# Kernel tuning notes

Measured on AMD Instinct MI355X. Metric: run time of the kernel, lower is better.

The kernel has to match this reference:

```python
import jax, jax.numpy as jnp
import numpy as np

D = 256          # embedding_dim
N_SUPPORT = 320  # n_way * n_shot = 20 * 16
N_QUERY = 2048
N_WAY = 20


def setup_inputs() -> dict:
    key = jax.random.key(0)
    ks = jax.random.split(key, 6)
    scale = 1.0 / np.sqrt(2 * D)
    return {
        "support_embeddings": jax.random.normal(ks[0], (N_SUPPORT, D), dtype=jnp.float32),
        "query_embeddings": jax.random.normal(ks[1], (N_QUERY, D), dtype=jnp.float32),
        "support_labels": jax.random.randint(ks[2], (N_SUPPORT,), 0, N_WAY, dtype=jnp.int64)
            if jax.config.jax_enable_x64 else jax.random.randint(ks[2], (N_SUPPORT,), 0, N_WAY, dtype=jnp.int32),
        "W1": jax.random.normal(ks[3], (2 * D, D), dtype=jnp.float32) * scale,
        "b1": jax.random.normal(ks[4], (D,), dtype=jnp.float32) * scale,
        "W2": jax.random.normal(ks[5], (D,), dtype=jnp.float32) * (1.0 / np.sqrt(D)),
        "b2": jnp.zeros((1,), dtype=jnp.float32),
        "n_way": N_WAY,
        "n_shot": 16,
    }


def reference(support_embeddings, query_embeddings, support_labels, W1, b1, W2, b2, n_way, n_shot):
    d = support_embeddings.shape[-1]
    # Linear1 over concat([query, support]) == query @ W1[:d] + support @ W1[d:]
    q_proj = query_embeddings @ W1[:d]          # [Q, D]
    s_proj = support_embeddings @ W1[d:]        # [S, D]
    hidden = jax.nn.relu(q_proj[:, None, :] + s_proj[None, :, :] + b1)  # [Q, S, D]
    scores = jnp.einsum("qsd,d->qs", hidden, W2) + b2[0]                # [Q, S]
    weights = jax.nn.softmax(scores, axis=1)                            # softmax over support set
    onehot = jax.nn.one_hot(support_labels, n_way, dtype=weights.dtype) # [S, n_way]
    logits = weights @ onehot                                           # [Q, n_way]
    return logits
```

## Files before the change

kernel.cpp:

```cpp
#include <hip/hip_runtime.h>
#include <cstdint>

#define DD   256
#define NS   320
#define NQ   2048
#define NWAY 20
#define QTP  8
#define QT   4
#define NQB  (NQ / QTP)
#define NSB  (NS / QTP)
#define CMAX 64

__global__ __launch_bounds__(1024) void proj_kernel(
    const float* __restrict__ sup, const float* __restrict__ qe,
    const float* __restrict__ W1, const float* __restrict__ b1,
    float* __restrict__ qp, float* __restrict__ spbT) {
  __shared__ float pacc[3][QTP][DD];
  const int t  = threadIdx.x;
  const int d  = t & 255;
  const int kq = t >> 8;
  const int b  = blockIdx.x;
  const bool isQ = (b < NQB);
  const int r0 = isQ ? b * QTP : (b - NQB) * QTP;
  const float* src   = isQ ? qe : sup;
  const float* wcol  = W1 + (isQ ? 0 : (size_t)DD * DD) + (size_t)(kq * 64) * DD + d;
  const float* rbase = src + __builtin_amdgcn_readfirstlane(r0 * DD + kq * 64);

  float acc[QTP] = {0.f, 0.f, 0.f, 0.f, 0.f, 0.f, 0.f, 0.f};
#pragma unroll 8
  for (int k = 0; k < 64; ++k) {
    const float wv = wcol[(size_t)k * DD];
#pragma unroll
    for (int i = 0; i < QTP; ++i)
      acc[i] += rbase[i * DD + k] * wv;
  }
  if (kq) {
#pragma unroll
    for (int i = 0; i < QTP; ++i) pacc[kq - 1][i][d] = acc[i];
  }
  __syncthreads();
  if (kq == 0) {
    if (isQ) {
#pragma unroll
      for (int i = 0; i < QTP; ++i)
        qp[(size_t)(r0 + i) * DD + d] =
            acc[i] + pacc[0][i][d] + pacc[1][i][d] + pacc[2][i][d];
    } else {
      const float bb = b1[d];
#pragma unroll
      for (int i = 0; i < QTP; ++i)
        spbT[d * NS + r0 + i] =
            acc[i] + pacc[0][i][d] + pacc[1][i][d] + pacc[2][i][d] + bb;
    }
  }
}

__global__ __launch_bounds__(640) void matchnet_kernel(
    const float* __restrict__ qp, const float* __restrict__ spbT,
    const float* __restrict__ W2, const int* __restrict__ labels,
    float* __restrict__ out) {
  __shared__ float wexp[QT][NS];
  __shared__ float wm[5];
  __shared__ float csum[QT * NWAY];
  __shared__ int   ccnt[NWAY];
  __shared__ short cidx[NWAY * CMAX];
  const int t    = threadIdx.x;
  const int q0   = blockIdx.x * QT;
  const int half = t / NS;
  const int s    = t - half * NS;

  if (t < NWAY) ccnt[t] = 0;
  __syncthreads();
  if (!half) {
    const int lab  = labels[s];
    const int slot = atomicAdd(&ccnt[lab], 1);
    cidx[lab * CMAX + slot] = (short)s;
  }

  const int d0 = half * (DD / 2);
  const float* qb = qp + __builtin_amdgcn_readfirstlane(q0 * DD + d0);
  const float* wb = W2 + d0;
  const float* sb = spbT + (size_t)d0 * NS + s;

  float acc[QT] = {0.f, 0.f, 0.f, 0.f};
#pragma unroll 4
  for (int dd = 0; dd < DD / 2; dd += 4) {
    const float sv0 = sb[(dd + 0) * NS];
    const float sv1 = sb[(dd + 1) * NS];
    const float sv2 = sb[(dd + 2) * NS];
    const float sv3 = sb[(dd + 3) * NS];
    const float4 wv = *(const float4*)(wb + dd);
#pragma unroll
    for (int i = 0; i < QT; ++i) {
      const float4 qv = *(const float4*)(qb + i * DD + dd);
      acc[i] += fmaxf(qv.x + sv0, 0.f) * wv.x
              + fmaxf(qv.y + sv1, 0.f) * wv.y
              + fmaxf(qv.z + sv2, 0.f) * wv.z
              + fmaxf(qv.w + sv3, 0.f) * wv.w;
    }
  }

  if (half) {
#pragma unroll
    for (int i = 0; i < QT; ++i) wexp[i][s] = acc[i];
  }
  __syncthreads();
  float m = -1e30f;
  if (!half) {
#pragma unroll
    for (int i = 0; i < QT; ++i) { acc[i] += wexp[i][s]; m = fmaxf(m, acc[i]); }
#pragma unroll
    for (int off = 32; off > 0; off >>= 1)
      m = fmaxf(m, __shfl_xor(m, off));
    if ((t & 63) == 0) wm[t >> 6] = m;
  }
  __syncthreads();
  if (!half) {
    const float M = fmaxf(fmaxf(fmaxf(wm[0], wm[1]), fmaxf(wm[2], wm[3])), wm[4]);
#pragma unroll
    for (int i = 0; i < QT; ++i) wexp[i][s] = __expf(acc[i] - M);
  }
  __syncthreads();
  if (t < QT * NWAY) {
    const int i = t / NWAY, c = t - i * NWAY;
    const int n = ccnt[c];
    float sum = 0.f;
    for (int j = 0; j < n; ++j) sum += wexp[i][cidx[c * CMAX + j]];
    csum[t] = sum;
  }
  __syncthreads();
  if (t < QT * NWAY) {
    const int i = t / NWAY, c = t - i * NWAY;
    float tot = 0.f;
#pragma unroll
    for (int j = 0; j < NWAY; ++j) tot += csum[i * NWAY + j];
    out[(size_t)(q0 + i) * NWAY + c] = csum[t] / tot;
  }
}

extern "C" void kernel_launch(void* const* d_in, const int* in_sizes, int n_in,
                              void* d_out, int out_size, void* d_ws, size_t ws_size,
                              hipStream_t stream) {
  const float* sup = (const float*)d_in[0];
  const float* qe  = (const float*)d_in[1];
  const int*   lab = (const int*)d_in[2];
  const float* W1  = (const float*)d_in[3];
  const float* b1  = (const float*)d_in[4];
  const float* W2  = (const float*)d_in[5];
  float* out  = (float*)d_out;
  float* spbT = (float*)d_ws;
  float* qpr  = spbT + (size_t)DD * NS;

  proj_kernel<<<NQB + NSB, 1024, 0, stream>>>(sup, qe, W1, b1, qpr, spbT);
  matchnet_kernel<<<NQ / QT, 640, 0, stream>>>(qpr, spbT, W2, lab, out);
}
```

Baseline: 101.0 us.

## Store projections in fp16 and use packed fp16 add/max with fdot2 in matchnet

```diff
diff --git a/kernel.cpp b/kernel.cpp
--- a/kernel.cpp
+++ b/kernel.cpp
@@ -11,10 +11,29 @@
 #define NSB  (NS / QTP)
 #define CMAX 64
 
+typedef _Float16 f16x2 __attribute__((ext_vector_type(2)));
+
+__device__ __forceinline__ f16x2 u2f(unsigned u) {
+  f16x2 f; __builtin_memcpy(&f, &u, 4); return f;
+}
+
+__device__ __forceinline__ float relu_dot2(f16x2 q, f16x2 s, f16x2 w, float c) {
+  f16x2 h = q + s;
+  const f16x2 z = {(_Float16)0.f, (_Float16)0.f};
+  h = __builtin_elementwise_max(h, z);
+#if __has_builtin(__builtin_amdgcn_fdot2)
+  return __builtin_amdgcn_fdot2(h, w, c, false);
+#else
+  return c + (float)h.x * (float)w.x + (float)h.y * (float)w.y;
+#endif
+}
+
 __global__ __launch_bounds__(1024) void proj_kernel(
     const float* __restrict__ sup, const float* __restrict__ qe,
     const float* __restrict__ W1, const float* __restrict__ b1,
-    float* __restrict__ qp, float* __restrict__ spbT) {
+    const float* __restrict__ W2,
+    _Float16* __restrict__ qph, f16x2* __restrict__ spb2,
+    _Float16* __restrict__ w2h) {
   __shared__ float pacc[3][QTP][DD];
   const int t  = threadIdx.x;
   const int d  = t & 255;
@@ -25,6 +44,8 @@
   const float* src   = isQ ? qe : sup;
   const float* wcol  = W1 + (isQ ? 0 : (size_t)DD * DD) + (size_t)(kq * 64) * DD + d;
   const float* rbase = src + __builtin_amdgcn_readfirstlane(r0 * DD + kq * 64);
+
+  if (b == 0 && kq == 0) w2h[d] = (_Float16)W2[d];
 
   float acc[QTP] = {0.f, 0.f, 0.f, 0.f, 0.f, 0.f, 0.f, 0.f};
 #pragma unroll 8
@@ -42,22 +63,28 @@
   if (kq == 0) {
     if (isQ) {
 #pragma unroll
-      for (int i = 0; i < QTP; ++i)
-        qp[(size_t)(r0 + i) * DD + d] =
-            acc[i] + pacc[0][i][d] + pacc[1][i][d] + pacc[2][i][d];
+      for (int i = 0; i < QTP; ++i) {
+        const float v = acc[i] + pacc[0][i][d] + pacc[1][i][d] + pacc[2][i][d];
+        qph[(size_t)(r0 + i) * DD + d] = (_Float16)v;
+      }
     } else {
       const float bb = b1[d];
 #pragma unroll
-      for (int i = 0; i < QTP; ++i)
-        spbT[d * NS + r0 + i] =
-            acc[i] + pacc[0][i][d] + pacc[1][i][d] + pacc[2][i][d] + bb;
+      for (int i = 0; i < QTP; ++i) {
+        const float v = acc[i] + pacc[0][i][d] + pacc[1][i][d] + pacc[2][i][d] + bb;
+        const float vh = __shfl_down(v, 1);
+        if (!(d & 1)) {
+          f16x2 p = {(_Float16)v, (_Float16)vh};
+          spb2[(size_t)(d >> 1) * NS + (r0 + i)] = p;
+        }
+      }
     }
   }
 }
 
 __global__ __launch_bounds__(640) void matchnet_kernel(
-    const float* __restrict__ qp, const float* __restrict__ spbT,
-    const float* __restrict__ W2, const int* __restrict__ labels,
+    const _Float16* __restrict__ qph, const f16x2* __restrict__ spb2,
+    const _Float16* __restrict__ w2h, const int* __restrict__ labels,
     float* __restrict__ out) {
   __shared__ float wexp[QT][NS];
   __shared__ float wm[5];
@@ -78,25 +105,29 @@
   }
 
   const int d0 = half * (DD / 2);
-  const float* qb = qp + __builtin_amdgcn_readfirstlane(q0 * DD + d0);
-  const float* wb = W2 + d0;
-  const float* sb = spbT + (size_t)d0 * NS + s;
+  const _Float16* qb = qph + __builtin_amdgcn_readfirstlane(q0 * DD + d0);
+  const _Float16* wb = w2h + d0;
+  const f16x2*    sb = spb2 + (size_t)(d0 >> 1) * NS + s;
 
   float acc[QT] = {0.f, 0.f, 0.f, 0.f};
-#pragma unroll 4
-  for (int dd = 0; dd < DD / 2; dd += 4) {
-    const float sv0 = sb[(dd + 0) * NS];
-    const float sv1 = sb[(dd + 1) * NS];
-    const float sv2 = sb[(dd + 2) * NS];
-    const float sv3 = sb[(dd + 3) * NS];
-    const float4 wv = *(const float4*)(wb + dd);
+#pragma unroll 2
+  for (int dd = 0; dd < DD / 2; dd += 8) {
+    const int dp = dd >> 1;
+    const f16x2 sv0 = sb[(dp + 0) * NS];
+    const f16x2 sv1 = sb[(dp + 1) * NS];
+    const f16x2 sv2 = sb[(dp + 2) * NS];
+    const f16x2 sv3 = sb[(dp + 3) * NS];
+    const uint4 wv = *reinterpret_cast<const uint4*>(wb + dd);
+    const f16x2 w0 = u2f(wv.x), w1 = u2f(wv.y), w2 = u2f(wv.z), w3 = u2f(wv.w);
 #pragma unroll
     for (int i = 0; i < QT; ++i) {
-      const float4 qv = *(const float4*)(qb + i * DD + dd);
-      acc[i] += fmaxf(qv.x + sv0, 0.f) * wv.x
-              + fmaxf(qv.y + sv1, 0.f) * wv.y
-              + fmaxf(qv.z + sv2, 0.f) * wv.z
-              + fmaxf(qv.w + sv3, 0.f) * wv.w;
+      const uint4 qv = *reinterpret_cast<const uint4*>(qb + i * DD + dd);
+      float a = acc[i];
+      a = relu_dot2(u2f(qv.x), sv0, w0, a);
+      a = relu_dot2(u2f(qv.y), sv1, w1, a);
+      a = relu_dot2(u2f(qv.z), sv2, w2, a);
+      a = relu_dot2(u2f(qv.w), sv3, w3, a);
+      acc[i] = a;
     }
   }
 
@@ -147,10 +178,12 @@
   const float* W1  = (const float*)d_in[3];
   const float* b1  = (const float*)d_in[4];
   const float* W2  = (const float*)d_in[5];
-  float* out  = (float*)d_out;
-  float* spbT = (float*)d_ws;
-  float* qpr  = spbT + (size_t)DD * NS;
+  float* out = (float*)d_out;
+  char* ws = (char*)d_ws;
+  f16x2*    spb2 = (f16x2*)ws;
+  _Float16* qph  = (_Float16*)(ws + 256 * 1024);
+  _Float16* w2h  = (_Float16*)(ws + 256 * 1024 + 1024 * 1024);
 
-  proj_kernel<<<NQB + NSB, 1024, 0, stream>>>(sup, qe, W1, b1, qpr, spbT);
-  matchnet_kernel<<<NQ / QT, 640, 0, stream>>>(qpr, spbT, W2, lab, out);
+  proj_kernel<<<NQB + NSB, 1024, 0, stream>>>(sup, qe, W1, b1, W2, qph, spb2, w2h);
+  matchnet_kernel<<<NQ / QT, 640, 0, stream>>>(qph, spb2, w2h, lab, out);
 }
```

New measurement: 94.47 us. 6.5% less time.
